# Kernel optimization log

Hardware: AMD Instinct MI355X
Metric: run time of the kernel (lower is better)

## Reference

```python
import jax, jax.numpy as jnp
import numpy as np

B, T, E, H = 4, 1024, 512, 8
DH = E // H  # head dim = 64


def setup_inputs() -> dict:
    key = jax.random.key(0)
    ks = jax.random.split(key, 6)
    s = 1.0 / np.sqrt(E)
    return {
        "q": jax.random.normal(ks[0], (B, T, E), dtype=jnp.float32),
        "kv": jax.random.normal(ks[1], (B, T, E), dtype=jnp.float32),
        "Wq": jax.random.normal(ks[2], (E, E), dtype=jnp.float32) * s,
        "Wk": jax.random.normal(ks[3], (E, E), dtype=jnp.float32) * s,
        "Wv": jax.random.normal(ks[4], (E, E), dtype=jnp.float32) * s,
        "Wo": jax.random.normal(ks[5], (E, E), dtype=jnp.float32) * s,
        "head_num": H,
    }


def _split_heads_dh(x, h):
    # einops 'b t (d h)' with h=head_num: head index is FASTEST in channel dim
    b, t, e = x.shape
    d = e // h
    return x.reshape(b, t, d, h).transpose(0, 3, 1, 2)  # (b, h, t, d)


def reference(q, kv, Wq, Wk, Wv, Wo, head_num):
    e = q.shape[-1]
    dk = (e // head_num) ** 0.5  # NOTE: multiplied, per original code

    qp = q @ Wq   # weights stored as (in, out); Linear(bias=False)
    kp = kv @ Wk
    vp = kv @ Wv

    query = _split_heads_dh(qp, head_num)  # (b, h, t, d)
    key = _split_heads_dh(kp, head_num)
    value = _split_heads_dh(vp, head_num)

    qf = jnp.fft.fftn(query, axes=(-2, -1))  # complex, over (t, d)
    kf = jnp.fft.fftn(key, axes=(-2, -1))

    # complex einsum, key NOT conjugated (faithful to torch source)
    energy = jnp.einsum("bhid,bhjd->bhij", qf, kf) * dk
    energy = jnp.fft.ifftn(energy, axes=(-2, -1)).real  # (b, h, t, t)

    attention = jax.nn.softmax(energy, axis=-1)
    out = jnp.einsum("bhij,bhjd->bhid", attention, value)  # (b, h, t, d)

    # einops 'b h t d -> b t (h d)': head index SLOWEST in output channel dim
    b, h, t, d = out.shape
    out = out.transpose(0, 2, 1, 3).reshape(b, t, h * d)
    return out @ Wo
```

## Files before the change

### kernel.cpp

```cpp
#include <hip/hip_runtime.h>
#include <math.h>

#define BB 4
#define TT 1024
#define EE 512
#define HH 8
#define DD 64
#define BT (BB * TT)

typedef _Float16 f16;
typedef __attribute__((ext_vector_type(8))) _Float16 f16x8;
typedef __attribute__((ext_vector_type(4))) float f32x4;

__global__ __launch_bounds__(256) void prep_k(
    const float* __restrict__ q, const float* __restrict__ kv,
    const float* __restrict__ Wq, const float* __restrict__ Wk,
    const float* __restrict__ Wv, const float* __restrict__ Wo,
    f16* __restrict__ wqh, f16* __restrict__ wql,
    f16* __restrict__ wkh, f16* __restrict__ wkl,
    f16* __restrict__ wvh, f16* __restrict__ woh,
    f16* __restrict__ qAhi, f16* __restrict__ qAlo,
    f16* __restrict__ kvAhi, f16* __restrict__ kvAlo) {
    const int t = threadIdx.x;
    const int y = blockIdx.y;
    if (y < 4) {
        int idx = blockIdx.x * 256 + t;
        int k = idx & (EE - 1);
        int n = idx >> 9;
        if (y == 0) {
            float v = Wq[k * EE + n] * 512.0f;
            f16 hi = (f16)v;
            wqh[n * EE + k] = hi;
            wql[n * EE + k] = (f16)(v - (float)hi);
        } else if (y == 1) {
            int d = n >> 3, h = n & 7;
            int sn = (((DD - d) & (DD - 1)) << 3) | h;
            float v = Wk[k * EE + sn];
            f16 hi = (f16)v;
            wkh[n * EE + k] = hi;
            wkl[n * EE + k] = (f16)(v - (float)hi);
        } else if (y == 2) {
            wvh[n * EE + k] = (f16)Wv[k * EE + n];
        } else {
            woh[n * EE + k] = (f16)Wo[k * EE + n];
        }
    } else {
        const float* src = (y == 4) ? q : kv;
        f16* dh = (y == 4) ? qAhi : kvAhi;
        f16* dl = (y == 4) ? qAlo : kvAlo;
        int base = (blockIdx.x * 256 + t) * 8;
        float4 a = *(const float4*)&src[base];
        float4 c = *(const float4*)&src[base + 4];
        float xs[8] = {a.x, a.y, a.z, a.w, c.x, c.y, c.z, c.w};
        f16x8 hi, lo;
#pragma unroll
        for (int e = 0; e < 8; ++e) {
            f16 hh = (f16)xs[e];
            hi[e] = hh;
            lo[e] = (f16)(xs[e] - (float)hh);
        }
        *(f16x8*)&dh[base] = hi;
        *(f16x8*)&dl[base] = lo;
    }
}

__global__ __launch_bounds__(256) void proj_k(
    const f16* __restrict__ qAhi, const f16* __restrict__ qAlo,
    const f16* __restrict__ kvAhi, const f16* __restrict__ kvAlo,
    const f16* __restrict__ wqh, const f16* __restrict__ wql,
    const f16* __restrict__ wkh, const f16* __restrict__ wkl,
    const f16* __restrict__ wvh,
    f16* __restrict__ qhi, f16* __restrict__ qlo,
    f16* __restrict__ khi, f16* __restrict__ klo, f16* __restrict__ vT) {
    __shared__ __align__(16) f16 Ah_s[2][128][40];
    __shared__ __align__(16) f16 Al_s[2][128][40];
    __shared__ __align__(16) f16 Wh_s[2][64][40];
    __shared__ __align__(16) f16 Wl_s[2][64][40];
    __shared__ __align__(16) f16 Wv_s[2][64][40];
    f16 (*Ep)[136] = reinterpret_cast<f16(*)[136]>(&Ah_s[0][0][0]);

    const int t = threadIdx.x;
    const int w = t >> 6, l = t & 63;
    const int wm = w >> 1, wn = w & 1;
    const int fr = l & 15, fc = l >> 4;
    const int m0b = blockIdx.x * 128;
    const int n0b = blockIdx.y * 64;
    const int z   = blockIdx.z;
    const int ar = t >> 1, ak = t & 1;
    const int wr = t >> 2, wc = t & 3;

    const f16* AH = z ? kvAhi : qAhi;
    const f16* AL = z ? kvAlo : qAlo;
    const f16* WH = z ? wkh : wqh;
    const f16* WL = z ? wkl : wql;

    f32x4 accK[4][2], accV[4][2];
#pragma unroll
    for (int i = 0; i < 4; ++i)
#pragma unroll
        for (int j = 0; j < 2; ++j) {
            accK[i][j] = f32x4{0.f, 0.f, 0.f, 0.f};
            accV[i][j] = f32x4{0.f, 0.f, 0.f, 0.f};
        }

    f16x8 ah8[2], al8[2], wh8, wl8, wv8;

    auto loadAB = [&](int k0) {
        size_t aoff = (size_t)(m0b + ar) * EE + k0 + ak * 16;
        ah8[0] = *(const f16x8*)&AH[aoff];
        ah8[1] = *(const f16x8*)&AH[aoff + 8];
        al8[0] = *(const f16x8*)&AL[aoff];
        al8[1] = *(const f16x8*)&AL[aoff + 8];
        size_t woff = (size_t)(n0b + wr) * EE + k0 + wc * 8;
        wh8 = *(const f16x8*)&WH[woff];
        wl8 = *(const f16x8*)&WL[woff];
        if (z) wv8 = *(const f16x8*)&wvh[woff];
    };
    auto stage = [&](int bf) {
        *(f16x8*)&Ah_s[bf][ar][ak * 16]     = ah8[0];
        *(f16x8*)&Ah_s[bf][ar][ak * 16 + 8] = ah8[1];
        *(f16x8*)&Al_s[bf][ar][ak * 16]     = al8[0];
        *(f16x8*)&Al_s[bf][ar][ak * 16 + 8] = al8[1];
        *(f16x8*)&Wh_s[bf][wr][wc * 8] = wh8;
        *(f16x8*)&Wl_s[bf][wr][wc * 8] = wl8;
        if (z) *(f16x8*)&Wv_s[bf][wr][wc * 8] = wv8;
    };

    loadAB(0);
    stage(0);
    __syncthreads();
    int cur = 0;
    for (int ks = 0; ks < 16; ++ks) {
        if (ks < 15) loadAB((ks + 1) * 32);
        f16x8 Ahf[4], Alf[4], Bh[2], Bl[2], Bv[2];
#pragma unroll
        for (int mi = 0; mi < 4; ++mi) {
            Ahf[mi] = *(const f16x8*)&Ah_s[cur][wm * 64 + mi * 16 + fr][fc * 8];
            Alf[mi] = *(const f16x8*)&Al_s[cur][wm * 64 + mi * 16 + fr][fc * 8];
        }
#pragma unroll
        for (int nj = 0; nj < 2; ++nj) {
            Bh[nj] = *(const f16x8*)&Wh_s[cur][wn * 32 + nj * 16 + fr][fc * 8];
            Bl[nj] = *(const f16x8*)&Wl_s[cur][wn * 32 + nj * 16 + fr][fc * 8];
            if (z) Bv[nj] = *(const f16x8*)&Wv_s[cur][wn * 32 + nj * 16 + fr][fc * 8];
        }
        __builtin_amdgcn_s_setprio(1);
#pragma unroll
        for (int mi = 0; mi < 4; ++mi)
#pragma unroll
            for (int nj = 0; nj < 2; ++nj) {
                accK[mi][nj] = __builtin_amdgcn_mfma_f32_16x16x32_f16(
                    Ahf[mi], Bh[nj], accK[mi][nj], 0, 0, 0);
                accK[mi][nj] = __builtin_amdgcn_mfma_f32_16x16x32_f16(
                    Ahf[mi], Bl[nj], accK[mi][nj], 0, 0, 0);
                accK[mi][nj] = __builtin_amdgcn_mfma_f32_16x16x32_f16(
                    Alf[mi], Bh[nj], accK[mi][nj], 0, 0, 0);
                if (z)
                    accV[mi][nj] = __builtin_amdgcn_mfma_f32_16x16x32_f16(
                        Ahf[mi], Bv[nj], accV[mi][nj], 0, 0, 0);
            }
        __builtin_amdgcn_s_setprio(0);
        if (ks < 15) stage(cur ^ 1);
        __syncthreads();
        cur ^= 1;
    }

    f16* dsthi = z ? khi : qhi;
    f16* dstlo = z ? klo : qlo;
#pragma unroll
    for (int mi = 0; mi < 4; ++mi)
#pragma unroll
        for (int nj = 0; nj < 2; ++nj)
#pragma unroll
            for (int r = 0; r < 4; ++r)
                Ep[wn * 32 + nj * 16 + fr][wm * 64 + mi * 16 + fc * 4 + r] =
                    (f16)accK[mi][nj][r];
    __syncthreads();
#pragma unroll
    for (int i = 0; i < 4; ++i) {
        int task = t * 4 + i;
        int mr = task >> 3, h = task & 7;
        f16x8 v;
#pragma unroll
        for (int d = 0; d < 8; ++d) v[d] = Ep[8 * d + h][mr];
        *(f16x8*)&dsthi[((size_t)h * BT + m0b + mr) * DD + (n0b >> 3)] = v;
    }
    __syncthreads();
#pragma unroll
    for (int mi = 0; mi < 4; ++mi)
#pragma unroll
        for (int nj = 0; nj < 2; ++nj)
#pragma unroll
            for (int r = 0; r < 4; ++r) {
                float x = accK[mi][nj][r];
                f16 hh = (f16)x;
                Ep[wn * 32 + nj * 16 + fr][wm * 64 + mi * 16 + fc * 4 + r] =
                    (f16)(x - (float)hh);
            }
    __syncthreads();
#pragma unroll
    for (int i = 0; i < 4; ++i) {
        int task = t * 4 + i;
        int mr = task >> 3, h = task & 7;
        f16x8 v;
#pragma unroll
        for (int d = 0; d < 8; ++d) v[d] = Ep[8 * d + h][mr];
        *(f16x8*)&dstlo[((size_t)h * BT + m0b + mr) * DD + (n0b >> 3)] = v;
    }
    if (z) {
        __syncthreads();
#pragma unroll
        for (int mi = 0; mi < 4; ++mi)
#pragma unroll
            for (int nj = 0; nj < 2; ++nj)
#pragma unroll
                for (int r = 0; r < 4; ++r)
                    Ep[wn * 32 + nj * 16 + fr][wm * 64 + mi * 16 + fc * 4 + r] =
                        (f16)accV[mi][nj][r];
        __syncthreads();
#pragma unroll
        for (int i = 0; i < 4; ++i) {
            int task = t * 4 + i;
            int mg = task & 15, nn = task >> 4;
            int h = nn & 7, dl = nn >> 3;
            f16x8 v = *(const f16x8*)&Ep[nn][mg * 8];
            *(f16x8*)&vT[((size_t)(h * DD + (n0b >> 3) + dl)) * BT +
                         m0b + mg * 8] = v;
        }
    }
}

__global__ __launch_bounds__(256) void outmm_k(const f16* __restrict__ Af,
                                               const f16* __restrict__ WThi,
                                               float* __restrict__ out) {
    __shared__ __align__(16) f16 Ah_s[2][64][72];
    __shared__ __align__(16) f16 Wh_s[2][64][72];

    const int t = threadIdx.x;
    const int w = t >> 6, l = t & 63;
    const int wm = w >> 1, wn = w & 1;
    const int fr = l & 15, fc = l >> 4;
    const int m0b = blockIdx.x * 64;
    const int n0b = blockIdx.y * 64;
    const int sr = t >> 2, sch = t & 3;

    f32x4 acc[2][2];
#pragma unroll
    for (int i = 0; i < 2; ++i)
#pragma unroll
        for (int j = 0; j < 2; ++j) acc[i][j] = f32x4{0.f, 0.f, 0.f, 0.f};

    f16x8 af[2], wf[2];
    auto loadAB = [&](int k0) {
#pragma unroll
        for (int i = 0; i < 2; ++i) {
            af[i] = *(const f16x8*)&Af[(size_t)(m0b + sr) * EE + k0 + sch * 16 + i * 8];
            wf[i] = *(const f16x8*)&WThi[(size_t)(n0b + sr) * EE + k0 + sch * 16 + i * 8];
        }
    };
    auto stage = [&](int bf) {
#pragma unroll
        for (int i = 0; i < 2; ++i) {
            *(f16x8*)&Ah_s[bf][sr][sch * 16 + i * 8] = af[i];
            *(f16x8*)&Wh_s[bf][sr][sch * 16 + i * 8] = wf[i];
        }
    };

    loadAB(0);
    stage(0);
    __syncthreads();
    int cur = 0;
    for (int ks = 0; ks < 8; ++ks) {
        if (ks < 7) loadAB((ks + 1) * 64);
        f16x8 Ahf[2][2], Bhf[2][2];
#pragma unroll
        for (int mi = 0; mi < 2; ++mi)
#pragma unroll
            for (int kb = 0; kb < 2; ++kb)
                Ahf[mi][kb] =
                    *(const f16x8*)&Ah_s[cur][wm * 32 + mi * 16 + fr][kb * 32 + fc * 8];
#pragma unroll
        for (int nj = 0; nj < 2; ++nj)
#pragma unroll
            for (int kb = 0; kb < 2; ++kb)
                Bhf[nj][kb] =
                    *(const f16x8*)&Wh_s[cur][wn * 32 + nj * 16 + fr][kb * 32 + fc * 8];
        __builtin_amdgcn_s_setprio(1);
#pragma unroll
        for (int mi = 0; mi < 2; ++mi)
#pragma unroll
            for (int nj = 0; nj < 2; ++nj)
#pragma unroll
                for (int kb = 0; kb < 2; ++kb)
                    acc[mi][nj] = __builtin_amdgcn_mfma_f32_16x16x32_f16(
                        Ahf[mi][kb], Bhf[nj][kb], acc[mi][nj], 0, 0, 0);
        __builtin_amdgcn_s_setprio(0);
        if (ks < 7) stage(cur ^ 1);
        __syncthreads();
        cur ^= 1;
    }

#pragma unroll
    for (int mi = 0; mi < 2; ++mi)
#pragma unroll
        for (int nj = 0; nj < 2; ++nj)
#pragma unroll
            for (int r = 0; r < 4; ++r)
                out[(size_t)(m0b + wm * 32 + mi * 16 + fc * 4 + r) * EE +
                    n0b + wn * 32 + nj * 16 + fr] = acc[mi][nj][r];
}

__global__ __launch_bounds__(256) void attn_mfma_k(const f16* __restrict__ qhiP,
    const f16* __restrict__ qloP, const f16* __restrict__ khiP,
    const f16* __restrict__ kloP, const f16* __restrict__ vTP,
    f16* __restrict__ ctx) {
    __shared__ __align__(16) f16 Khi[2][64][64];
    __shared__ __align__(16) f16 Klo[2][64][64];
    __shared__ __align__(16) f16 Pl[4][16][88];

    const int bid = blockIdx.x;
    const int swz = (bid & 7) * 64 + (bid >> 3);
    const int bx = swz & 15;
    const int h  = (swz >> 4) & 7;
    const int b  = swz >> 7;

    const int t  = threadIdx.x;
    const int w  = t >> 6;
    const int l  = t & 63;
    const int lg = l >> 4;
    const int lq = l & 15;
    const int q0 = bx * 64 + w * 16;
    const size_t plane = ((size_t)h * BT + (size_t)b * TT) * DD;

    f16x8 Qhi[2], Qlo[2];
#pragma unroll
    for (int kf = 0; kf < 2; ++kf) {
        size_t qo = plane + (size_t)(q0 + lq) * DD + kf * 32 + lg * 8;
        Qhi[kf] = *(const f16x8*)&qhiP[qo];
        Qlo[kf] = *(const f16x8*)&qloP[qo];
    }
    const f16* vbase = vTP + ((size_t)h * DD + lq) * BT + (size_t)b * TT + lg * 8;

    f32x4 Oacc[4];
#pragma unroll
    for (int i = 0; i < 4; ++i) Oacc[i] = f32x4{0.f, 0.f, 0.f, 0.f};
    float m = -1e30f, lsum = 0.f;

    const int sr = t >> 2, sch = t & 3;
    f16x8 kh[2], kl[2];

    auto loadK = [&](int kt0) {
        size_t off = plane + (size_t)(kt0 + sr) * DD + sch * 16;
        kh[0] = *(const f16x8*)&khiP[off];
        kh[1] = *(const f16x8*)&khiP[off + 8];
        kl[0] = *(const f16x8*)&kloP[off];
        kl[1] = *(const f16x8*)&kloP[off + 8];
    };
    auto stageK = [&](int bf) {
#pragma unroll
        for (int i = 0; i < 2; ++i) {
            int chunk = sch * 2 + i;
            int dsw = chunk ^ (sr & 7);
            *(f16x8*)&Khi[bf][sr][dsw * 8] = kh[i];
            *(f16x8*)&Klo[bf][sr][dsw * 8] = kl[i];
        }
    };

    loadK(0);
    stageK(0);
    __syncthreads();
    int cur = 0;

    for (int kt0 = 0; kt0 < TT; kt0 += 64) {
        f16x8 bv[2][4];
#pragma unroll
        for (int kf = 0; kf < 2; ++kf)
#pragma unroll
            for (int dvt = 0; dvt < 4; ++dvt)
                bv[kf][dvt] = *(const f16x8*)&vbase[(size_t)dvt * 16 * BT +
                                                    kt0 + kf * 32];
        if (kt0 + 64 < TT) loadK(kt0 + 64);

        f32x4 Sc[4];
        __builtin_amdgcn_s_setprio(1);
#pragma unroll
        for (int kt = 0; kt < 4; ++kt) {
            f32x4 c = f32x4{0.f, 0.f, 0.f, 0.f};
            int keyr = kt * 16 + lq;
#pragma unroll
            for (int kf = 0; kf < 2; ++kf) {
                int dblk = kf * 4 + lg;
                int sw = dblk ^ (keyr & 7);
                f16x8 ahi = *(const f16x8*)&Khi[cur][keyr][sw * 8];
                f16x8 alo = *(const f16x8*)&Klo[cur][keyr][sw * 8];
                c = __builtin_amdgcn_mfma_f32_16x16x32_f16(ahi, Qhi[kf], c, 0, 0, 0);
                c = __builtin_amdgcn_mfma_f32_16x16x32_f16(ahi, Qlo[kf], c, 0, 0, 0);
                c = __builtin_amdgcn_mfma_f32_16x16x32_f16(alo, Qhi[kf], c, 0, 0, 0);
            }
            Sc[kt] = c;
        }
        __builtin_amdgcn_s_setprio(0);

        float s[16];
#pragma unroll
        for (int kt = 0; kt < 4; ++kt)
#pragma unroll
            for (int r = 0; r < 4; ++r) s[kt * 4 + r] = Sc[kt][r];
        float tm = s[0];
#pragma unroll
        for (int i = 1; i < 16; ++i) tm = fmaxf(tm, s[i]);
        tm = fmaxf(tm, __shfl_xor(tm, 16));
        tm = fmaxf(tm, __shfl_xor(tm, 32));

        bool skip = __all(tm <= m + 8.0f);
        float Mn = m, corr = 1.0f;
        if (!skip) {
            Mn = fmaxf(m, tm);
            corr = __expf(m - Mn);
        }
        float ps = 0.f;
        f16 ph[16];
#pragma unroll
        for (int i = 0; i < 16; ++i) {
            float p = __expf(s[i] - Mn);
            ps += p;
            ph[i] = (f16)p;
        }
        ps += __shfl_xor(ps, 16);
        ps += __shfl_xor(ps, 32);
        if (skip) {
            lsum += ps;
        } else {
            lsum = lsum * corr + ps;
            m = Mn;
        }

#pragma unroll
        for (int kt = 0; kt < 4; ++kt)
#pragma unroll
            for (int rp = 0; rp < 4; rp += 2) {
                union { f16 h; unsigned short u; } u0, u1;
                u0.h = ph[kt * 4 + rp]; u1.h = ph[kt * 4 + rp + 1];
                unsigned int pk = ((unsigned int)u1.u << 16) | u0.u;
                *(unsigned int*)&Pl[w][lq][kt * 16 + lg * 4 + rp] = pk;
            }

        if (!skip) {
            float cq[4];
#pragma unroll
            for (int r = 0; r < 4; ++r) cq[r] = __shfl(corr, lg * 4 + r);
#pragma unroll
            for (int dvt = 0; dvt < 4; ++dvt)
#pragma unroll
                for (int r = 0; r < 4; ++r) Oacc[dvt][r] *= cq[r];
        }

        __builtin_amdgcn_s_setprio(1);
#pragma unroll
        for (int kf = 0; kf < 2; ++kf) {
            f16x8 pa = *(const f16x8*)&Pl[w][lq][kf * 32 + lg * 8];
#pragma unroll
            for (int dvt = 0; dvt < 4; ++dvt)
                Oacc[dvt] = __builtin_amdgcn_mfma_f32_16x16x32_f16(
                    pa, bv[kf][dvt], Oacc[dvt], 0, 0, 0);
        }
        __builtin_amdgcn_s_setprio(0);

        if (kt0 + 64 < TT) stageK(cur ^ 1);
        __syncthreads();
        cur ^= 1;
    }

    float linv = 1.0f / lsum;
    float lq4[4];
#pragma unroll
    for (int r = 0; r < 4; ++r) lq4[r] = __shfl(linv, lg * 4 + r);
#pragma unroll
    for (int r = 0; r < 4; ++r) {
        f16* crow = ctx + (size_t)(b * TT + q0 + lg * 4 + r) * EE + h * DD;
#pragma unroll
        for (int dvt = 0; dvt < 4; ++dvt)
            crow[dvt * 16 + lq] = (f16)(Oacc[dvt][r] * lq4[r]);
    }
}

extern "C" void kernel_launch(void* const* d_in, const int* in_sizes, int n_in,
                              void* d_out, int out_size, void* d_ws, size_t ws_size,
                              hipStream_t stream) {
    const float* q  = (const float*)d_in[0];
    const float* kv = (const float*)d_in[1];
    const float* Wq = (const float*)d_in[2];
    const float* Wk = (const float*)d_in[3];
    const float* Wv = (const float*)d_in[4];
    const float* Wo = (const float*)d_in[5];
    float* out = (float*)d_out;

    f16* ws = (f16*)d_ws;
    const size_t PL  = (size_t)HH * BT * DD;
    const size_t WPL = (size_t)EE * EE;
    f16* qhi   = ws + 0 * PL;
    f16* qlo   = ws + 1 * PL;
    f16* khi   = ws + 2 * PL;
    f16* klo   = ws + 3 * PL;
    f16* vT    = ws + 4 * PL;
    f16* ctx   = ws + 5 * PL;
    f16* qAhi  = ws + 6 * PL;
    f16* qAlo  = ws + 7 * PL;
    f16* kvAhi = ws + 8 * PL;
    f16* kvAlo = ws + 9 * PL;
    f16* wqh = ws + 10 * PL;
    f16* wql = wqh + 1 * WPL;
    f16* wkh = wqh + 2 * WPL;
    f16* wkl = wqh + 3 * WPL;
    f16* wvh = wqh + 4 * WPL;
    f16* woh = wqh + 5 * WPL;

    prep_k<<<dim3(1024, 6), dim3(256), 0, stream>>>(
        q, kv, Wq, Wk, Wv, Wo, wqh, wql, wkh, wkl, wvh, woh,
        qAhi, qAlo, kvAhi, kvAlo);

    proj_k<<<dim3(BT / 128, EE / 64, 2), dim3(256), 0, stream>>>(
        qAhi, qAlo, kvAhi, kvAlo, wqh, wql, wkh, wkl, wvh,
        qhi, qlo, khi, klo, vT);

    attn_mfma_k<<<dim3(512), dim3(256), 0, stream>>>(
        qhi, qlo, khi, klo, vT, ctx);

    outmm_k<<<dim3(BT / 64, EE / 64), dim3(256), 0, stream>>>(ctx, woh, out);
}
```

Measured before the change: 82.98 us.

## Split attention over key halves with a separate combine kernel

Splits the key dimension of the attention kernel into two halves, doubling the grid from 512 to 1024 blocks so more of the GPU's compute units stay busy. Each block writes unnormalized fp32 partial outputs plus its running max and sum, and a new combine kernel merges the two halves with log-sum-exp weights into the fp16 context buffer. This costs an extra kernel launch and extra global memory traffic for the fp32 partials. The P staging buffer padding also shrinks from 88 to 72.

```diff
diff --git a/kernel.cpp b/kernel.cpp
--- a/kernel.cpp
+++ b/kernel.cpp
@@ -310,19 +310,20 @@
                     n0b + wn * 32 + nj * 16 + fr] = acc[mi][nj][r];
 }
 
-__global__ __launch_bounds__(256) void attn_mfma_k(const f16* __restrict__ qhiP,
+__global__ __launch_bounds__(256) void attn_part_k(const f16* __restrict__ qhiP,
     const f16* __restrict__ qloP, const f16* __restrict__ khiP,
     const f16* __restrict__ kloP, const f16* __restrict__ vTP,
-    f16* __restrict__ ctx) {
+    float* __restrict__ Opart, float* __restrict__ mlP) {
     __shared__ __align__(16) f16 Khi[2][64][64];
     __shared__ __align__(16) f16 Klo[2][64][64];
-    __shared__ __align__(16) f16 Pl[4][16][88];
+    __shared__ __align__(16) f16 Pl[4][16][72];
 
     const int bid = blockIdx.x;
-    const int swz = (bid & 7) * 64 + (bid >> 3);
+    const int swz = (bid & 7) * 128 + (bid >> 3);
     const int bx = swz & 15;
-    const int h  = (swz >> 4) & 7;
-    const int b  = swz >> 7;
+    const int s  = (swz >> 4) & 1;
+    const int h  = (swz >> 5) & 7;
+    const int b  = swz >> 8;
 
     const int t  = threadIdx.x;
     const int w  = t >> 6;
@@ -366,12 +367,13 @@
         }
     };
 
-    loadK(0);
+    const int k_beg = s * 512, k_end = k_beg + 512;
+    loadK(k_beg);
     stageK(0);
     __syncthreads();
     int cur = 0;
 
-    for (int kt0 = 0; kt0 < TT; kt0 += 64) {
+    for (int kt0 = k_beg; kt0 < k_end; kt0 += 64) {
         f16x8 bv[2][4];
 #pragma unroll
         for (int kf = 0; kf < 2; ++kf)
@@ -379,7 +381,7 @@
             for (int dvt = 0; dvt < 4; ++dvt)
                 bv[kf][dvt] = *(const f16x8*)&vbase[(size_t)dvt * 16 * BT +
                                                     kt0 + kf * 32];
-        if (kt0 + 64 < TT) loadK(kt0 + 64);
+        if (kt0 + 64 < k_end) loadK(kt0 + 64);
 
         f32x4 Sc[4];
         __builtin_amdgcn_s_setprio(1);
@@ -401,14 +403,14 @@
         }
         __builtin_amdgcn_s_setprio(0);
 
-        float s[16];
+        float sv[16];
 #pragma unroll
         for (int kt = 0; kt < 4; ++kt)
 #pragma unroll
-            for (int r = 0; r < 4; ++r) s[kt * 4 + r] = Sc[kt][r];
-        float tm = s[0];
-#pragma unroll
-        for (int i = 1; i < 16; ++i) tm = fmaxf(tm, s[i]);
+            for (int r = 0; r < 4; ++r) sv[kt * 4 + r] = Sc[kt][r];
+        float tm = sv[0];
+#pragma unroll
+        for (int i = 1; i < 16; ++i) tm = fmaxf(tm, sv[i]);
         tm = fmaxf(tm, __shfl_xor(tm, 16));
         tm = fmaxf(tm, __shfl_xor(tm, 32));
 
@@ -422,7 +424,7 @@
         f16 ph[16];
 #pragma unroll
         for (int i = 0; i < 16; ++i) {
-            float p = __expf(s[i] - Mn);
+            float p = __expf(sv[i] - Mn);
             ps += p;
             ph[i] = (f16)p;
         }
@@ -466,22 +468,54 @@
         }
         __builtin_amdgcn_s_setprio(0);
 
-        if (kt0 + 64 < TT) stageK(cur ^ 1);
+        if (kt0 + 64 < k_end) stageK(cur ^ 1);
         __syncthreads();
         cur ^= 1;
     }
 
-    float linv = 1.0f / lsum;
-    float lq4[4];
-#pragma unroll
-    for (int r = 0; r < 4; ++r) lq4[r] = __shfl(linv, lg * 4 + r);
+    const size_t rowbase = (size_t)(s * HH + h) * BT + (size_t)b * TT + q0;
+    if (lg == 0) {
+        mlP[(rowbase + lq) * 2]     = m;
+        mlP[(rowbase + lq) * 2 + 1] = lsum;
+    }
 #pragma unroll
     for (int r = 0; r < 4; ++r) {
-        f16* crow = ctx + (size_t)(b * TT + q0 + lg * 4 + r) * EE + h * DD;
+        float* orow = Opart + (rowbase + lg * 4 + r) * DD;
 #pragma unroll
         for (int dvt = 0; dvt < 4; ++dvt)
-            crow[dvt * 16 + lq] = (f16)(Oacc[dvt][r] * lq4[r]);
-    }
+            orow[dvt * 16 + lq] = Oacc[dvt][r];
+    }
+}
+
+__global__ __launch_bounds__(256) void comb_k(const float* __restrict__ Op,
+                                              const float* __restrict__ ml,
+                                              f16* __restrict__ ctx) {
+    int task = blockIdx.x * 256 + threadIdx.x;
+    int d8 = task & 7;
+    int gq = (task >> 3) & (BT - 1);
+    int h  = task >> 15;
+    size_t r1 = (size_t)h * BT + gq;
+    size_t r2 = (size_t)(HH + h) * BT + gq;
+    float m1 = ml[r1 * 2], l1 = ml[r1 * 2 + 1];
+    float m2 = ml[r2 * 2], l2 = ml[r2 * 2 + 1];
+    float M = fmaxf(m1, m2);
+    float w1 = __expf(m1 - M), w2 = __expf(m2 - M);
+    float inv = 1.0f / (l1 * w1 + l2 * w2);
+    w1 *= inv; w2 *= inv;
+    const float4* o1 = (const float4*)&Op[r1 * DD + d8 * 8];
+    const float4* o2 = (const float4*)&Op[r2 * DD + d8 * 8];
+    float4 a1 = o1[0], b1 = o1[1];
+    float4 a2 = o2[0], b2 = o2[1];
+    f16x8 o;
+    o[0] = (f16)(a1.x * w1 + a2.x * w2);
+    o[1] = (f16)(a1.y * w1 + a2.y * w2);
+    o[2] = (f16)(a1.z * w1 + a2.z * w2);
+    o[3] = (f16)(a1.w * w1 + a2.w * w2);
+    o[4] = (f16)(b1.x * w1 + b2.x * w2);
+    o[5] = (f16)(b1.y * w1 + b2.y * w2);
+    o[6] = (f16)(b1.z * w1 + b2.z * w2);
+    o[7] = (f16)(b1.w * w1 + b2.w * w2);
+    *(f16x8*)&ctx[(size_t)gq * EE + h * DD + d8 * 8] = o;
 }
 
 extern "C" void kernel_launch(void* const* d_in, const int* in_sizes, int n_in,
@@ -514,6 +548,8 @@
     f16* wkl = wqh + 3 * WPL;
     f16* wvh = wqh + 4 * WPL;
     f16* woh = wqh + 5 * WPL;
+    float* Opart = (float*)(wqh + 6 * WPL);
+    float* mlP   = Opart + (size_t)2 * HH * BT * DD;
 
     prep_k<<<dim3(1024, 6), dim3(256), 0, stream>>>(
         q, kv, Wq, Wk, Wv, Wo, wqh, wql, wkh, wkl, wvh, woh,
@@ -523,8 +559,10 @@
         qAhi, qAlo, kvAhi, kvAlo, wqh, wql, wkh, wkl, wvh,
         qhi, qlo, khi, klo, vT);
 
-    attn_mfma_k<<<dim3(512), dim3(256), 0, stream>>>(
-        qhi, qlo, khi, klo, vT, ctx);
+    attn_part_k<<<dim3(1024), dim3(256), 0, stream>>>(
+        qhi, qlo, khi, klo, vT, Opart, mlP);
+
+    comb_k<<<dim3(1024), dim3(256), 0, stream>>>(Opart, mlP, ctx);
 
     outmm_k<<<dim3(BT / 64, EE / 64), dim3(256), 0, stream>>>(ctx, woh, out);
 }
```

Result: slower. 95.31 us (+14.9%).
